# Performance work log

Hardware: AMD Instinct MI355X
Metric: run time of the kernel (lower is better)

## Reference

```python
import jax, jax.numpy as jnp
import numpy as np

B, L, D, K_LIN, T = 32, 512, 1024, 7, 8  # T = 1 identity ('root') + 7 linear experts


def setup_inputs() -> dict:
    key = jax.random.key(0)
    k0, k1, k2 = jax.random.split(key, 3)
    actions = jax.random.normal(k0, (B, L, D), dtype=jnp.float32)
    action_type = jax.random.randint(k1, (B, L), 0, T)
    W = jax.random.normal(k2, (K_LIN, D, D), dtype=jnp.float32) * 0.02  # (K, out, in)
    b = jnp.zeros((K_LIN, D), dtype=jnp.float32)
    return {"actions": actions, "action_type": action_type, "W": W, "b": b}


def reference(actions, action_type, W, b):
    # Project padded actions through ALL experts (matches original ModuleDict loop).
    # proj: (B, L, K_LIN, D) ; W is (K, out, in) so contract over input dim i.
    proj = jnp.einsum('bli,koi->blko', actions, W) + b[None, None, :, :]
    # 'root' expert is nn.Identity -> stacked first (dict insertion order).
    p = jnp.concatenate([actions[:, :, None, :], proj], axis=2)  # (B, L, T, D)
    # One-hot mask built via scatter in the original == one_hot here.
    mask = jax.nn.one_hot(action_type, T, dtype=p.dtype)[..., None]  # (B, L, T, 1)
    embedded = (mask * p).sum(axis=2)  # (B, L, D)
    return embedded
```

## Files before the change

kernel.cpp:

```cpp
#include <hip/hip_runtime.h>


#define NTOK 16384
#define DDIM 1024
#define NEXP 7
#define BM 256
#define BN 256
#define BK 64
#define NKT (DDIM / BK)

#define WI_OFFS   16
#define WI_NTILES 32
#define WI_TABLE  64
#define WI_CTOK   512
#define WS_ABF_B  1048576
#define WS_WBF_B  (WS_ABF_B + NTOK * DDIM * 2)

typedef __attribute__((ext_vector_type(8))) short short8;
typedef __attribute__((ext_vector_type(4))) float f32x4;

__device__ __forceinline__ unsigned short f2bf(float f) {
    unsigned u = __float_as_uint(f);
    u += 0x7fff + ((u >> 16) & 1);
    return (unsigned short)(u >> 16);
}

__device__ __forceinline__ void gload16(const void* g, void* l) {
    __builtin_amdgcn_global_load_lds(
        (const __attribute__((address_space(1))) void*)g,
        (__attribute__((address_space(3))) void*)l, 16, 0, 0);
}

__global__ __launch_bounds__(1024) void prep_k(
    const int* __restrict__ type, int* __restrict__ wsi,
    const float* __restrict__ W, unsigned short* __restrict__ Wbf,
    const float* __restrict__ A, unsigned short* __restrict__ Abf,
    float* __restrict__ out) {
    const int bid = blockIdx.x, tid = threadIdx.x;
    if (bid == 0) {
        __shared__ int h[16][8];
        __shared__ int base2[16][8];
        const int wave = tid >> 6, lane = tid & 63;
        const unsigned long long lt = (1ULL << lane) - 1;

        const int4* tsrc = (const int4*)(type + tid * 16);
        int4 v0 = tsrc[0], v1 = tsrc[1], v2 = tsrc[2], v3 = tsrc[3];
        int kv[16] = { v0.x, v0.y, v0.z, v0.w, v1.x, v1.y, v1.z, v1.w,
                       v2.x, v2.y, v2.z, v2.w, v3.x, v3.y, v3.z, v3.w };

        int cnt[8];
#pragma unroll
        for (int e = 0; e < 8; ++e) cnt[e] = 0;
#pragma unroll
        for (int i = 0; i < 16; ++i) {
#pragma unroll
            for (int e = 1; e < 8; ++e)
                cnt[e] += __popcll(__ballot(kv[i] == e));
        }
        if (lane == 0) {
#pragma unroll
            for (int e = 0; e < 8; ++e) h[wave][e] = cnt[e];
        }
        __syncthreads();

        if (tid == 0) {
            int acc = 0, t = 0;
            for (int e = 0; e < NEXP; ++e) {
                wsi[WI_OFFS + e] = acc;
                int run = acc;
                for (int w = 0; w < 16; ++w) { base2[w][e + 1] = run; run += h[w][e + 1]; }
                int nt = (run - acc + BM - 1) >> 8;
                for (int i = 0; i < nt; ++i) {
                    wsi[WI_TABLE + 2 * t] = e;
                    wsi[WI_TABLE + 2 * t + 1] = acc + i * BM;
                    ++t;
                }
                acc = run;
            }
            wsi[WI_OFFS + NEXP] = acc;
            wsi[WI_NTILES] = t;
        }
        __syncthreads();

        int rb[8];
#pragma unroll
        for (int e = 1; e < 8; ++e) rb[e] = base2[wave][e];
#pragma unroll
        for (int i = 0; i < 16; ++i) {
            int k = kv[i];
            int pos = -1;
#pragma unroll
            for (int e = 1; e < 8; ++e) {
                unsigned long long m = __ballot(k == e);
                int p = rb[e] + __popcll(m & lt);
                pos = (k == e) ? p : pos;
                rb[e] += __popcll(m);
            }
            if (k > 0) wsi[WI_CTOK + pos] = tid * 16 + i;
        }
    } else if (bid <= 448) {
        size_t i = ((size_t)(bid - 1) * 1024 + tid) * 16;
        const float4* src = (const float4*)(W + i);
        float4 v0 = src[0], v1 = src[1], v2 = src[2], v3 = src[3];
        short8 h0, h1;
        h0[0]=f2bf(v0.x); h0[1]=f2bf(v0.y); h0[2]=f2bf(v0.z); h0[3]=f2bf(v0.w);
        h0[4]=f2bf(v1.x); h0[5]=f2bf(v1.y); h0[6]=f2bf(v1.z); h0[7]=f2bf(v1.w);
        h1[0]=f2bf(v2.x); h1[1]=f2bf(v2.y); h1[2]=f2bf(v2.z); h1[3]=f2bf(v2.w);
        h1[4]=f2bf(v3.x); h1[5]=f2bf(v3.y); h1[6]=f2bf(v3.z); h1[7]=f2bf(v3.w);
        *(short8*)(Wbf + i) = h0;
        *(short8*)(Wbf + i + 8) = h1;
    } else {
        const int wave = tid >> 6, lane = tid & 63;
        const int t = (bid - 449) * 16 + wave;
        const float4* src = (const float4*)(A + (size_t)t * DDIM);
        if (type[t] == 0) {
            float4* d = (float4*)(out + (size_t)t * DDIM);
#pragma unroll
            for (int j = 0; j < 4; ++j) d[lane + j * 64] = src[lane + j * 64];
        } else {
            float4 v0 = src[lane * 4 + 0], v1 = src[lane * 4 + 1];
            float4 v2 = src[lane * 4 + 2], v3 = src[lane * 4 + 3];
            short8 h0, h1;
            h0[0]=f2bf(v0.x); h0[1]=f2bf(v0.y); h0[2]=f2bf(v0.z); h0[3]=f2bf(v0.w);
            h0[4]=f2bf(v1.x); h0[5]=f2bf(v1.y); h0[6]=f2bf(v1.z); h0[7]=f2bf(v1.w);
            h1[0]=f2bf(v2.x); h1[1]=f2bf(v2.y); h1[2]=f2bf(v2.z); h1[3]=f2bf(v2.w);
            h1[4]=f2bf(v3.x); h1[5]=f2bf(v3.y); h1[6]=f2bf(v3.z); h1[7]=f2bf(v3.w);
            unsigned short* d = Abf + (size_t)t * DDIM + lane * 16;
            *(short8*)d = h0;
            *(short8*)(d + 8) = h1;
        }
    }
}

#define TILE(Abase, Bbase, sNA, sNB, KT)                           \
    do {                                                           \
        short8 a1[8], b1[4];                                       \
        _Pragma("unroll")                                          \
        for (int m = 0; m < 8; ++m)                                \
            a1[m] = *(const short8*)(Abase + sl0 + m * 2048);      \
        _Pragma("unroll")                                          \
        for (int n = 0; n < 4; ++n)                                \
            b1[n] = *(const short8*)(Bbase + sl0 + n * 2048);      \
        if ((KT) + 1 < NKT) {                                      \
            const int ke_ = ((KT) + 1) * BK;                       \
            _Pragma("unroll")                                      \
            for (int q = 0; q < 4; ++q)                            \
                gload16(aSrc[q] + ke_, sNA + q * 8192);            \
            _Pragma("unroll")                                      \
            for (int q = 0; q < 4; ++q)                            \
                gload16(bSrc[q] + ke_, sNB + q * 8192);            \
        }                                                          \
        __builtin_amdgcn_s_setprio(1);                             \
        _Pragma("unroll")                                          \
        for (int m = 0; m < 8; ++m)                                \
            _Pragma("unroll")                                      \
            for (int n = 0; n < 4; ++n)                            \
                acc[m][n] = __builtin_amdgcn_mfma_f32_16x16x32_bf16(\
                    a1[m], b1[n], acc[m][n], 0, 0, 0);             \
        __builtin_amdgcn_s_setprio(0);                             \
        short8 a2[8], b2[4];                                       \
        _Pragma("unroll")                                          \
        for (int m = 0; m < 8; ++m)                                \
            a2[m] = *(const short8*)(Abase + sl1 + m * 2048);      \
        _Pragma("unroll")                                          \
        for (int n = 0; n < 4; ++n)                                \
            b2[n] = *(const short8*)(Bbase + sl1 + n * 2048);      \
        __builtin_amdgcn_s_setprio(1);                             \
        _Pragma("unroll")                                          \
        for (int m = 0; m < 8; ++m)                                \
            _Pragma("unroll")                                      \
            for (int n = 0; n < 4; ++n)                            \
                acc[m][n] = __builtin_amdgcn_mfma_f32_16x16x32_bf16(\
                    a2[m], b2[n], acc[m][n], 0, 0, 0);             \
        __builtin_amdgcn_s_setprio(0);                             \
        asm volatile("s_waitcnt vmcnt(0)" ::: "memory");           \
        __builtin_amdgcn_s_barrier();                              \
    } while (0)

__global__ __launch_bounds__(512, 2) void gemm_k(
    const unsigned short* __restrict__ Abf,
    const unsigned short* __restrict__ Wbf,
    const float* __restrict__ bias, float* __restrict__ out,
    const int* __restrict__ wsi) {
    const int bid = blockIdx.x;
    const int c = bid & 7;
    const int g = bid >> 3;
    const int ntiles = wsi[WI_NTILES];
    const int* offs = wsi + WI_OFFS;
    const int* tab  = wsi + WI_TABLE;
    const int* ctok = wsi + WI_CTOK;
    const int nlin  = offs[NEXP];

    __shared__ unsigned short As0[BM * BK];
    __shared__ unsigned short As1[BM * BK];
    __shared__ unsigned short Bs0[BM * BK];
    __shared__ unsigned short Bs1[BM * BK];

    const int tid = threadIdx.x, lane = tid & 63, wave = tid >> 6;
    const int wr = wave >> 2, wc = wave & 3;
    const int lane15 = lane & 15;
    const int srow = lane >> 3;
    const int schunk = ((lane & 7) ^ srow) * 8;

    const int sl0 = (((lane >> 4)) ^ (lane & 7)) * 16;
    const int sl1 = ((4 | (lane >> 4)) ^ (lane & 7)) * 16;
    const char* aR0 = (const char*)As0 + wr * 16384 + lane15 * 128;
    const char* aR1 = (const char*)As1 + wr * 16384 + lane15 * 128;
    const char* bR0 = (const char*)Bs0 + wc * 8192 + lane15 * 128;
    const char* bR1 = (const char*)Bs1 + wc * 8192 + lane15 * 128;
    char* sA0 = (char*)As0 + wave * 1024;
    char* sA1 = (char*)As1 + wave * 1024;
    char* sB0 = (char*)Bs0 + wave * 1024;
    char* sB1 = (char*)Bs1 + wave * 1024;

    for (int rep = 0; rep < 2; ++rep) {
        const int q4 = g + 32 * rep;
        const int ty = (q4 >> 2) * 8 + c;
        const int tx = q4 & 3;
        if (ty >= ntiles) break;

        const int e     = tab[2 * ty];
        const int crow0 = tab[2 * ty + 1];
        const int nend  = offs[e + 1];
        const int col0  = tx * BN;
        const unsigned short* Wb = Wbf + (size_t)e * DDIM * DDIM;

        const unsigned short* aSrc[4];
        const unsigned short* bSrc[4];
#pragma unroll
        for (int q = 0; q < 4; ++q) {
            int r = min(crow0 + q * 64 + wave * 8 + srow, nlin - 1);
            aSrc[q] = Abf + (size_t)ctok[r] * DDIM + schunk;
            bSrc[q] = Wb + (size_t)(col0 + q * 64 + wave * 8 + srow) * DDIM + schunk;
        }

        f32x4 acc[8][4];
#pragma unroll
        for (int m = 0; m < 8; ++m)
#pragma unroll
            for (int n = 0; n < 4; ++n) acc[m][n] = (f32x4){0.f, 0.f, 0.f, 0.f};

#pragma unroll
        for (int q = 0; q < 4; ++q) gload16(aSrc[q], sA0 + q * 8192);
#pragma unroll
        for (int q = 0; q < 4; ++q) gload16(bSrc[q], sB0 + q * 8192);
        asm volatile("s_waitcnt vmcnt(0)" ::: "memory");
        __builtin_amdgcn_s_barrier();

        for (int kt2 = 0; kt2 < NKT / 2; ++kt2) {
            TILE(aR0, bR0, sA1, sB1, 2 * kt2);
            TILE(aR1, bR1, sA0, sB0, 2 * kt2 + 1);
        }

        const int crow4 = (lane >> 4) * 4;
        float bv[4];
#pragma unroll
        for (int n = 0; n < 4; ++n)
            bv[n] = bias[e * DDIM + col0 + wc * 64 + n * 16 + lane15];

#pragma unroll
        for (int m = 0; m < 8; ++m) {
#pragma unroll
            for (int r = 0; r < 4; ++r) {
                int gr = crow0 + wr * 128 + m * 16 + crow4 + r;
                if (gr >= nend) continue;
                int tok = ctok[gr];
                float* orow = out + (size_t)tok * DDIM + col0 + wc * 64 + lane15;
#pragma unroll
                for (int n = 0; n < 4; ++n)
                    orow[n * 16] = acc[m][n][r] + bv[n];
            }
        }
        __builtin_amdgcn_s_barrier();
    }
}

extern "C" void kernel_launch(void* const* d_in, const int* in_sizes, int n_in,
                              void* d_out, int out_size, void* d_ws, size_t ws_size,
                              hipStream_t stream) {
    const float* actions = (const float*)d_in[0];
    const int*   atype   = (const int*)d_in[1];
    const float* W       = (const float*)d_in[2];
    const float* bias    = (const float*)d_in[3];
    float* out = (float*)d_out;

    int* wsi = (int*)d_ws;
    unsigned short* Abf = (unsigned short*)((char*)d_ws + WS_ABF_B);
    unsigned short* Wbf = (unsigned short*)((char*)d_ws + WS_WBF_B);

    prep_k<<<1473, 1024, 0, stream>>>(atype, wsi, W, Wbf, actions, Abf, out);
    gemm_k<<<256, 512, 0, stream>>>(Abf, Wbf, bias, out, wsi);
}
```

Measured before the change: 69.44 us.

## Restructure GEMM main loop into 4-phase pipeline with fine-grained staging

Replaces the two-half K-tile loop with four MFMA phases per tile, each covering a quadrant of the output (4 M-rows by 2 N-cols). Global-to-LDS loads are split into per-quadrant chunks that prefetch up to two tiles ahead, and partial vmcnt waits replace full drains. The aim is to overlap global loads, LDS reads and MFMA more finely and cut full-barrier stalls. It adds extra barriers per phase and relies on correct ordering of partial waits and buffer reuse across the two LDS buffers.

After: 73.10 us. 5.3% more time.

```diff
diff --git a/kernel.cpp b/kernel.cpp
--- a/kernel.cpp
+++ b/kernel.cpp
@@ -132,49 +132,65 @@
     }
 }
 
-#define TILE(Abase, Bbase, sNA, sNB, KT)                           \
-    do {                                                           \
-        short8 a1[8], b1[4];                                       \
-        _Pragma("unroll")                                          \
-        for (int m = 0; m < 8; ++m)                                \
-            a1[m] = *(const short8*)(Abase + sl0 + m * 2048);      \
-        _Pragma("unroll")                                          \
-        for (int n = 0; n < 4; ++n)                                \
-            b1[n] = *(const short8*)(Bbase + sl0 + n * 2048);      \
-        if ((KT) + 1 < NKT) {                                      \
-            const int ke_ = ((KT) + 1) * BK;                       \
-            _Pragma("unroll")                                      \
-            for (int q = 0; q < 4; ++q)                            \
-                gload16(aSrc[q] + ke_, sNA + q * 8192);            \
-            _Pragma("unroll")                                      \
-            for (int q = 0; q < 4; ++q)                            \
-                gload16(bSrc[q] + ke_, sNB + q * 8192);            \
-        }                                                          \
-        __builtin_amdgcn_s_setprio(1);                             \
-        _Pragma("unroll")                                          \
-        for (int m = 0; m < 8; ++m)                                \
-            _Pragma("unroll")                                      \
-            for (int n = 0; n < 4; ++n)                            \
-                acc[m][n] = __builtin_amdgcn_mfma_f32_16x16x32_bf16(\
-                    a1[m], b1[n], acc[m][n], 0, 0, 0);             \
-        __builtin_amdgcn_s_setprio(0);                             \
-        short8 a2[8], b2[4];                                       \
-        _Pragma("unroll")                                          \
-        for (int m = 0; m < 8; ++m)                                \
-            a2[m] = *(const short8*)(Abase + sl1 + m * 2048);      \
-        _Pragma("unroll")                                          \
-        for (int n = 0; n < 4; ++n)                                \
-            b2[n] = *(const short8*)(Bbase + sl1 + n * 2048);      \
-        __builtin_amdgcn_s_setprio(1);                             \
-        _Pragma("unroll")                                          \
-        for (int m = 0; m < 8; ++m)                                \
-            _Pragma("unroll")                                      \
-            for (int n = 0; n < 4; ++n)                            \
-                acc[m][n] = __builtin_amdgcn_mfma_f32_16x16x32_bf16(\
-                    a2[m], b2[n], acc[m][n], 0, 0, 0);             \
-        __builtin_amdgcn_s_setprio(0);                             \
-        asm volatile("s_waitcnt vmcnt(0)" ::: "memory");           \
-        __builtin_amdgcn_s_barrier();                              \
+#define RD_A(AR, MQ)                                                \
+    _Pragma("unroll")                                               \
+    for (int i = 0; i < 4; ++i) {                                   \
+        a[i][0] = *(const short8*)((AR) + ((MQ) * 4 + i) * 2048 + sl0); \
+        a[i][1] = *(const short8*)((AR) + ((MQ) * 4 + i) * 2048 + sl1); \
+    }
+
+#define RD_B(BR, NP)                                                \
+    _Pragma("unroll")                                               \
+    for (int n = 0; n < 2; ++n) {                                   \
+        b[n][0] = *(const short8*)((BR) + ((NP) * 2 + n) * 2048 + sl0); \
+        b[n][1] = *(const short8*)((BR) + ((NP) * 2 + n) * 2048 + sl1); \
+    }
+
+#define STG_A(DST, MQ, KTT)                                         \
+    gload16(aP[MQ][0] + (KTT) * BK, (char*)(DST) + dA[MQ][0]);      \
+    gload16(aP[MQ][1] + (KTT) * BK, (char*)(DST) + dA[MQ][1]);
+
+#define STG_B(DST, NP, KTT)                                         \
+    gload16(bP[NP][0] + (KTT) * BK, (char*)(DST) + dB[NP][0]);      \
+    gload16(bP[NP][1] + (KTT) * BK, (char*)(DST) + dB[NP][1]);
+
+#define MF_PH(MQ, NP)                                               \
+    __builtin_amdgcn_s_barrier();                                   \
+    asm volatile("s_waitcnt lgkmcnt(0)" ::: "memory");              \
+    __builtin_amdgcn_sched_barrier(0);                              \
+    __builtin_amdgcn_s_setprio(1);                                  \
+    _Pragma("unroll")                                               \
+    for (int i = 0; i < 4; ++i)                                     \
+        _Pragma("unroll")                                           \
+        for (int n = 0; n < 2; ++n) {                               \
+            acc[(MQ)*4+i][(NP)*2+n] = __builtin_amdgcn_mfma_f32_16x16x32_bf16( \
+                a[i][0], b[n][0], acc[(MQ)*4+i][(NP)*2+n], 0, 0, 0);\
+            acc[(MQ)*4+i][(NP)*2+n] = __builtin_amdgcn_mfma_f32_16x16x32_bf16( \
+                a[i][1], b[n][1], acc[(MQ)*4+i][(NP)*2+n], 0, 0, 0);\
+        }                                                           \
+    __builtin_amdgcn_s_setprio(0);                                  \
+    __builtin_amdgcn_s_barrier();
+
+#define TILE8(AR, BR, AD, BD, BDN, KT)                              \
+    do {                                                            \
+        short8 a[4][2], b[2][2];                                    \
+        RD_A(AR, 0); RD_B(BR, 0);                                   \
+        if ((KT) + 1 < NKT) { STG_B(BDN, 0, (KT) + 1); }            \
+        MF_PH(0, 0);                                                \
+        RD_B(BR, 1);                                                \
+        if ((KT) + 2 < NKT) { STG_A(AD, 0, (KT) + 2); }             \
+        MF_PH(0, 1);                                                \
+        RD_A(AR, 1);                                                \
+        if ((KT) + 2 < NKT) { STG_B(BD, 1, (KT) + 2); }             \
+        MF_PH(1, 1);                                                \
+        RD_B(BR, 0);                                                \
+        if ((KT) + 2 < NKT) {                                       \
+            STG_A(AD, 1, (KT) + 2);                                 \
+            asm volatile("s_waitcnt vmcnt(6)" ::: "memory");        \
+        } else {                                                    \
+            asm volatile("s_waitcnt vmcnt(0)" ::: "memory");        \
+        }                                                           \
+        MF_PH(1, 0);                                                \
     } while (0)
 
 __global__ __launch_bounds__(512, 2) void gemm_k(
@@ -199,8 +215,8 @@
     const int tid = threadIdx.x, lane = tid & 63, wave = tid >> 6;
     const int wr = wave >> 2, wc = wave & 3;
     const int lane15 = lane & 15;
-    const int srow = lane >> 3;
-    const int schunk = ((lane & 7) ^ srow) * 8;
+    const int l3 = lane >> 3;
+    const int schunk = ((lane & 7) ^ l3) * 8;
 
     const int sl0 = (((lane >> 4)) ^ (lane & 7)) * 16;
     const int sl1 = ((4 | (lane >> 4)) ^ (lane & 7)) * 16;
@@ -208,10 +224,18 @@
     const char* aR1 = (const char*)As1 + wr * 16384 + lane15 * 128;
     const char* bR0 = (const char*)Bs0 + wc * 8192 + lane15 * 128;
     const char* bR1 = (const char*)Bs1 + wc * 8192 + lane15 * 128;
-    char* sA0 = (char*)As0 + wave * 1024;
-    char* sA1 = (char*)As1 + wave * 1024;
-    char* sB0 = (char*)Bs0 + wave * 1024;
-    char* sB1 = (char*)Bs1 + wave * 1024;
+
+    int dA[2][2], dB[2][2];
+#pragma unroll
+    for (int mq = 0; mq < 2; ++mq)
+#pragma unroll
+        for (int j = 0; j < 2; ++j)
+            dA[mq][j] = (j * 128 + mq * 64 + wave * 8) * 128;
+#pragma unroll
+    for (int np = 0; np < 2; ++np)
+#pragma unroll
+        for (int j = 0; j < 2; ++j)
+            dB[np][j] = ((((wave >> 2) + 2 * j) * 64) + np * 32 + (wave & 3) * 8) * 128;
 
     for (int rep = 0; rep < 2; ++rep) {
         const int q4 = g + 32 * rep;
@@ -225,14 +249,17 @@
         const int col0  = tx * BN;
         const unsigned short* Wb = Wbf + (size_t)e * DDIM * DDIM;
 
-        const unsigned short* aSrc[4];
-        const unsigned short* bSrc[4];
-#pragma unroll
-        for (int q = 0; q < 4; ++q) {
-            int r = min(crow0 + q * 64 + wave * 8 + srow, nlin - 1);
-            aSrc[q] = Abf + (size_t)ctok[r] * DDIM + schunk;
-            bSrc[q] = Wb + (size_t)(col0 + q * 64 + wave * 8 + srow) * DDIM + schunk;
-        }
+        const unsigned short* aP[2][2];
+        const unsigned short* bP[2][2];
+#pragma unroll
+        for (int mq = 0; mq < 2; ++mq)
+#pragma unroll
+            for (int j = 0; j < 2; ++j) {
+                int r = j * 128 + mq * 64 + wave * 8 + l3;
+                aP[mq][j] = Abf + (size_t)ctok[min(crow0 + r, nlin - 1)] * DDIM + schunk;
+                int cc = ((wave >> 2) + 2 * j) * 64 + mq * 32 + (wave & 3) * 8 + l3;
+                bP[mq][j] = Wb + (size_t)(col0 + cc) * DDIM + schunk;
+            }
 
         f32x4 acc[8][4];
 #pragma unroll
@@ -240,16 +267,14 @@
 #pragma unroll
             for (int n = 0; n < 4; ++n) acc[m][n] = (f32x4){0.f, 0.f, 0.f, 0.f};
 
-#pragma unroll
-        for (int q = 0; q < 4; ++q) gload16(aSrc[q], sA0 + q * 8192);
-#pragma unroll
-        for (int q = 0; q < 4; ++q) gload16(bSrc[q], sB0 + q * 8192);
-        asm volatile("s_waitcnt vmcnt(0)" ::: "memory");
+        STG_A(As0, 0, 0); STG_B(Bs0, 0, 0); STG_B(Bs0, 1, 0); STG_A(As0, 1, 0);
+        STG_A(As1, 0, 1); STG_B(Bs1, 1, 1); STG_A(As1, 1, 1);
+        asm volatile("s_waitcnt vmcnt(6)" ::: "memory");
         __builtin_amdgcn_s_barrier();
 
         for (int kt2 = 0; kt2 < NKT / 2; ++kt2) {
-            TILE(aR0, bR0, sA1, sB1, 2 * kt2);
-            TILE(aR1, bR1, sA0, sB0, 2 * kt2 + 1);
+            TILE8(aR0, bR0, As0, Bs0, Bs1, 2 * kt2);
+            TILE8(aR1, bR1, As1, Bs1, Bs0, 2 * kt2 + 1);
         }
 
         const int crow4 = (lane >> 4) * 4;
```

## Fuse prep and grouped GEMM into one persistent kernel with grid barrier

Applied to the files above, without the earlier changes.

Merges the routing/conversion prep kernel and the grouped expert GEMM into a single 256-block kernel. Block 0 does the token bucketing, the other blocks grid-stride over the weight and activation bf16 conversion work, and then every block meets at an atomic grid-wide barrier before running the GEMM. This removes one kernel launch and the gap between the two kernels. In exchange it adds a memset for the barrier counter and relies on all 256 blocks being resident at once. The conversion phase now runs on far fewer threads (256x512 instead of 1473x1024), which may lower the memory bandwidth it reaches.

New measurement: 102.7 us. +47.9%, slower.

```diff
diff --git a/kernel.cpp b/kernel.cpp
--- a/kernel.cpp
+++ b/kernel.cpp
@@ -9,6 +9,7 @@
 #define BK 64
 #define NKT (DDIM / BK)
 
+#define WI_BAR    0
 #define WI_OFFS   16
 #define WI_NTILES 32
 #define WI_TABLE  64
@@ -29,107 +30,6 @@
     __builtin_amdgcn_global_load_lds(
         (const __attribute__((address_space(1))) void*)g,
         (__attribute__((address_space(3))) void*)l, 16, 0, 0);
-}
-
-__global__ __launch_bounds__(1024) void prep_k(
-    const int* __restrict__ type, int* __restrict__ wsi,
-    const float* __restrict__ W, unsigned short* __restrict__ Wbf,
-    const float* __restrict__ A, unsigned short* __restrict__ Abf,
-    float* __restrict__ out) {
-    const int bid = blockIdx.x, tid = threadIdx.x;
-    if (bid == 0) {
-        __shared__ int h[16][8];
-        __shared__ int base2[16][8];
-        const int wave = tid >> 6, lane = tid & 63;
-        const unsigned long long lt = (1ULL << lane) - 1;
-
-        const int4* tsrc = (const int4*)(type + tid * 16);
-        int4 v0 = tsrc[0], v1 = tsrc[1], v2 = tsrc[2], v3 = tsrc[3];
-        int kv[16] = { v0.x, v0.y, v0.z, v0.w, v1.x, v1.y, v1.z, v1.w,
-                       v2.x, v2.y, v2.z, v2.w, v3.x, v3.y, v3.z, v3.w };
-
-        int cnt[8];
-#pragma unroll
-        for (int e = 0; e < 8; ++e) cnt[e] = 0;
-#pragma unroll
-        for (int i = 0; i < 16; ++i) {
-#pragma unroll
-            for (int e = 1; e < 8; ++e)
-                cnt[e] += __popcll(__ballot(kv[i] == e));
-        }
-        if (lane == 0) {
-#pragma unroll
-            for (int e = 0; e < 8; ++e) h[wave][e] = cnt[e];
-        }
-        __syncthreads();
-
-        if (tid == 0) {
-            int acc = 0, t = 0;
-            for (int e = 0; e < NEXP; ++e) {
-                wsi[WI_OFFS + e] = acc;
-                int run = acc;
-                for (int w = 0; w < 16; ++w) { base2[w][e + 1] = run; run += h[w][e + 1]; }
-                int nt = (run - acc + BM - 1) >> 8;
-                for (int i = 0; i < nt; ++i) {
-                    wsi[WI_TABLE + 2 * t] = e;
-                    wsi[WI_TABLE + 2 * t + 1] = acc + i * BM;
-                    ++t;
-                }
-                acc = run;
-            }
-            wsi[WI_OFFS + NEXP] = acc;
-            wsi[WI_NTILES] = t;
-        }
-        __syncthreads();
-
-        int rb[8];
-#pragma unroll
-        for (int e = 1; e < 8; ++e) rb[e] = base2[wave][e];
-#pragma unroll
-        for (int i = 0; i < 16; ++i) {
-            int k = kv[i];
-            int pos = -1;
-#pragma unroll
-            for (int e = 1; e < 8; ++e) {
-                unsigned long long m = __ballot(k == e);
-                int p = rb[e] + __popcll(m & lt);
-                pos = (k == e) ? p : pos;
-                rb[e] += __popcll(m);
-            }
-            if (k > 0) wsi[WI_CTOK + pos] = tid * 16 + i;
-        }
-    } else if (bid <= 448) {
-        size_t i = ((size_t)(bid - 1) * 1024 + tid) * 16;
-        const float4* src = (const float4*)(W + i);
-        float4 v0 = src[0], v1 = src[1], v2 = src[2], v3 = src[3];
-        short8 h0, h1;
-        h0[0]=f2bf(v0.x); h0[1]=f2bf(v0.y); h0[2]=f2bf(v0.z); h0[3]=f2bf(v0.w);
-        h0[4]=f2bf(v1.x); h0[5]=f2bf(v1.y); h0[6]=f2bf(v1.z); h0[7]=f2bf(v1.w);
-        h1[0]=f2bf(v2.x); h1[1]=f2bf(v2.y); h1[2]=f2bf(v2.z); h1[3]=f2bf(v2.w);
-        h1[4]=f2bf(v3.x); h1[5]=f2bf(v3.y); h1[6]=f2bf(v3.z); h1[7]=f2bf(v3.w);
-        *(short8*)(Wbf + i) = h0;
-        *(short8*)(Wbf + i + 8) = h1;
-    } else {
-        const int wave = tid >> 6, lane = tid & 63;
-        const int t = (bid - 449) * 16 + wave;
-        const float4* src = (const float4*)(A + (size_t)t * DDIM);
-        if (type[t] == 0) {
-            float4* d = (float4*)(out + (size_t)t * DDIM);
-#pragma unroll
-            for (int j = 0; j < 4; ++j) d[lane + j * 64] = src[lane + j * 64];
-        } else {
-            float4 v0 = src[lane * 4 + 0], v1 = src[lane * 4 + 1];
-            float4 v2 = src[lane * 4 + 2], v3 = src[lane * 4 + 3];
-            short8 h0, h1;
-            h0[0]=f2bf(v0.x); h0[1]=f2bf(v0.y); h0[2]=f2bf(v0.z); h0[3]=f2bf(v0.w);
-            h0[4]=f2bf(v1.x); h0[5]=f2bf(v1.y); h0[6]=f2bf(v1.z); h0[7]=f2bf(v1.w);
-            h1[0]=f2bf(v2.x); h1[1]=f2bf(v2.y); h1[2]=f2bf(v2.z); h1[3]=f2bf(v2.w);
-            h1[4]=f2bf(v3.x); h1[5]=f2bf(v3.y); h1[6]=f2bf(v3.z); h1[7]=f2bf(v3.w);
-            unsigned short* d = Abf + (size_t)t * DDIM + lane * 16;
-            *(short8*)d = h0;
-            *(short8*)(d + 8) = h1;
-        }
-    }
 }
 
 #define TILE(Abase, Bbase, sNA, sNB, KT)                           \
@@ -177,12 +77,127 @@
         __builtin_amdgcn_s_barrier();                              \
     } while (0)
 
-__global__ __launch_bounds__(512, 2) void gemm_k(
-    const unsigned short* __restrict__ Abf,
-    const unsigned short* __restrict__ Wbf,
-    const float* __restrict__ bias, float* __restrict__ out,
-    const int* __restrict__ wsi) {
-    const int bid = blockIdx.x;
+__global__ __launch_bounds__(512, 2) void fused_k(
+    const int* __restrict__ type, int* __restrict__ wsi,
+    const float* __restrict__ W, unsigned short* __restrict__ Wbf,
+    const float* __restrict__ A, unsigned short* __restrict__ Abf,
+    const float* __restrict__ bias, float* __restrict__ out) {
+    const int bid = blockIdx.x, tid = threadIdx.x;
+    const int lane = tid & 63, wave = tid >> 6;
+
+    __shared__ unsigned short As0[BM * BK];
+    __shared__ unsigned short As1[BM * BK];
+    __shared__ unsigned short Bs0[BM * BK];
+    __shared__ unsigned short Bs1[BM * BK];
+    __shared__ int h[8][8];
+    __shared__ int base2[8][8];
+
+    if (bid == 0) {
+        const unsigned long long lt = (1ULL << lane) - 1;
+        const int4* tsrc = (const int4*)(type + tid * 32);
+        int4 v[8];
+#pragma unroll
+        for (int j = 0; j < 8; ++j) v[j] = tsrc[j];
+        int kv[32];
+#pragma unroll
+        for (int j = 0; j < 8; ++j) {
+            kv[4 * j + 0] = v[j].x; kv[4 * j + 1] = v[j].y;
+            kv[4 * j + 2] = v[j].z; kv[4 * j + 3] = v[j].w;
+        }
+        int cnt[8];
+#pragma unroll
+        for (int e = 0; e < 8; ++e) cnt[e] = 0;
+#pragma unroll
+        for (int i = 0; i < 32; ++i) {
+#pragma unroll
+            for (int e = 1; e < 8; ++e)
+                cnt[e] += __popcll(__ballot(kv[i] == e));
+        }
+        if (lane == 0) {
+#pragma unroll
+            for (int e = 0; e < 8; ++e) h[wave][e] = cnt[e];
+        }
+        __syncthreads();
+        if (tid == 0) {
+            int acc = 0, t = 0;
+            for (int e = 0; e < NEXP; ++e) {
+                wsi[WI_OFFS + e] = acc;
+                int run = acc;
+                for (int w = 0; w < 8; ++w) { base2[w][e + 1] = run; run += h[w][e + 1]; }
+                int nt = (run - acc + BM - 1) >> 8;
+                for (int i = 0; i < nt; ++i) {
+                    wsi[WI_TABLE + 2 * t] = e;
+                    wsi[WI_TABLE + 2 * t + 1] = acc + i * BM;
+                    ++t;
+                }
+                acc = run;
+            }
+            wsi[WI_OFFS + NEXP] = acc;
+            wsi[WI_NTILES] = t;
+        }
+        __syncthreads();
+        int rb[8];
+#pragma unroll
+        for (int e = 1; e < 8; ++e) rb[e] = base2[wave][e];
+#pragma unroll
+        for (int i = 0; i < 32; ++i) {
+            int k = kv[i];
+            int pos = -1;
+#pragma unroll
+            for (int e = 1; e < 8; ++e) {
+                unsigned long long m = __ballot(k == e);
+                int p = rb[e] + __popcll(m & lt);
+                pos = (k == e) ? p : pos;
+                rb[e] += __popcll(m);
+            }
+            if (k > 0) wsi[WI_CTOK + pos] = tid * 32 + i;
+        }
+    } else {
+        for (int u = bid - 1; u < 2944; u += 255) {
+            if (u < 896) {
+                size_t i = (size_t)u * 8192 + tid * 16;
+                const float4* src = (const float4*)(W + i);
+                float4 v0 = src[0], v1 = src[1], v2 = src[2], v3 = src[3];
+                short8 h0, h1;
+                h0[0]=f2bf(v0.x); h0[1]=f2bf(v0.y); h0[2]=f2bf(v0.z); h0[3]=f2bf(v0.w);
+                h0[4]=f2bf(v1.x); h0[5]=f2bf(v1.y); h0[6]=f2bf(v1.z); h0[7]=f2bf(v1.w);
+                h1[0]=f2bf(v2.x); h1[1]=f2bf(v2.y); h1[2]=f2bf(v2.z); h1[3]=f2bf(v2.w);
+                h1[4]=f2bf(v3.x); h1[5]=f2bf(v3.y); h1[6]=f2bf(v3.z); h1[7]=f2bf(v3.w);
+                *(short8*)(Wbf + i) = h0;
+                *(short8*)(Wbf + i + 8) = h1;
+            } else {
+                const int t = (u - 896) * 8 + wave;
+                const float4* src = (const float4*)(A + (size_t)t * DDIM);
+                if (type[t] == 0) {
+                    float4* d = (float4*)(out + (size_t)t * DDIM);
+#pragma unroll
+                    for (int j = 0; j < 4; ++j) d[lane + j * 64] = src[lane + j * 64];
+                } else {
+                    float4 v0 = src[lane * 4 + 0], v1 = src[lane * 4 + 1];
+                    float4 v2 = src[lane * 4 + 2], v3 = src[lane * 4 + 3];
+                    short8 h0, h1;
+                    h0[0]=f2bf(v0.x); h0[1]=f2bf(v0.y); h0[2]=f2bf(v0.z); h0[3]=f2bf(v0.w);
+                    h0[4]=f2bf(v1.x); h0[5]=f2bf(v1.y); h0[6]=f2bf(v1.z); h0[7]=f2bf(v1.w);
+                    h1[0]=f2bf(v2.x); h1[1]=f2bf(v2.y); h1[2]=f2bf(v2.z); h1[3]=f2bf(v2.w);
+                    h1[4]=f2bf(v3.x); h1[5]=f2bf(v3.y); h1[6]=f2bf(v3.z); h1[7]=f2bf(v3.w);
+                    unsigned short* d = Abf + (size_t)t * DDIM + lane * 16;
+                    *(short8*)d = h0;
+                    *(short8*)(d + 8) = h1;
+                }
+            }
+        }
+    }
+
+    __syncthreads();
+    if (tid == 0) {
+        __hip_atomic_fetch_add(&wsi[WI_BAR], 1, __ATOMIC_RELEASE,
+                               __HIP_MEMORY_SCOPE_AGENT);
+        while (__hip_atomic_load(&wsi[WI_BAR], __ATOMIC_ACQUIRE,
+                                 __HIP_MEMORY_SCOPE_AGENT) < 256)
+            __builtin_amdgcn_s_sleep(8);
+    }
+    __syncthreads();
+
     const int c = bid & 7;
     const int g = bid >> 3;
     const int ntiles = wsi[WI_NTILES];
@@ -191,12 +206,6 @@
     const int* ctok = wsi + WI_CTOK;
     const int nlin  = offs[NEXP];
 
-    __shared__ unsigned short As0[BM * BK];
-    __shared__ unsigned short As1[BM * BK];
-    __shared__ unsigned short Bs0[BM * BK];
-    __shared__ unsigned short Bs1[BM * BK];
-
-    const int tid = threadIdx.x, lane = tid & 63, wave = tid >> 6;
     const int wr = wave >> 2, wc = wave & 3;
     const int lane15 = lane & 15;
     const int srow = lane >> 3;
@@ -288,6 +297,7 @@
     unsigned short* Abf = (unsigned short*)((char*)d_ws + WS_ABF_B);
     unsigned short* Wbf = (unsigned short*)((char*)d_ws + WS_WBF_B);
 
-    prep_k<<<1473, 1024, 0, stream>>>(atype, wsi, W, Wbf, actions, Abf, out);
-    gemm_k<<<256, 512, 0, stream>>>(Abf, Wbf, bias, out, wsi);
+    hipMemsetAsync(d_ws, 0, 64, stream);
+    fused_k<<<256, 512, 0, stream>>>(atype, wsi, W, Wbf, actions, Abf,
+                                     bias, out);
 }
```

## Fuse activation bf16 conversion into GEMM A-tile loading

Applied to the files above, without the earlier changes.

Removes the separate pass in the prep kernel that converted gathered activations to a bf16 workspace buffer. The GEMM now reads fp32 activations directly into registers, converts them to bf16 and writes them into swizzled LDS, while B tiles still use direct global-to-LDS loads. This saves one fp32 read plus one bf16 write and read of the activation matrix. In exchange it adds register pressure (launch bounds drop to one block per CU), ALU conversion work and an extra LDS wait inside the main loop, and each A tile is re-read from global as fp32 by all four column-tile blocks.

Result: slower. 94.84 us (+36.6%).

```diff
diff --git a/kernel.cpp b/kernel.cpp
--- a/kernel.cpp
+++ b/kernel.cpp
@@ -13,8 +13,7 @@
 #define WI_NTILES 32
 #define WI_TABLE  64
 #define WI_CTOK   512
-#define WS_ABF_B  1048576
-#define WS_WBF_B  (WS_ABF_B + NTOK * DDIM * 2)
+#define WS_WBF_B  1048576
 
 typedef __attribute__((ext_vector_type(8))) short short8;
 typedef __attribute__((ext_vector_type(4))) float f32x4;
@@ -34,8 +33,7 @@
 __global__ __launch_bounds__(1024) void prep_k(
     const int* __restrict__ type, int* __restrict__ wsi,
     const float* __restrict__ W, unsigned short* __restrict__ Wbf,
-    const float* __restrict__ A, unsigned short* __restrict__ Abf,
-    float* __restrict__ out) {
+    const float* __restrict__ A, float* __restrict__ out) {
     const int bid = blockIdx.x, tid = threadIdx.x;
     if (bid == 0) {
         __shared__ int h[16][8];
@@ -112,29 +110,19 @@
     } else {
         const int wave = tid >> 6, lane = tid & 63;
         const int t = (bid - 449) * 16 + wave;
-        const float4* src = (const float4*)(A + (size_t)t * DDIM);
         if (type[t] == 0) {
+            const float4* src = (const float4*)(A + (size_t)t * DDIM);
             float4* d = (float4*)(out + (size_t)t * DDIM);
 #pragma unroll
             for (int j = 0; j < 4; ++j) d[lane + j * 64] = src[lane + j * 64];
-        } else {
-            float4 v0 = src[lane * 4 + 0], v1 = src[lane * 4 + 1];
-            float4 v2 = src[lane * 4 + 2], v3 = src[lane * 4 + 3];
-            short8 h0, h1;
-            h0[0]=f2bf(v0.x); h0[1]=f2bf(v0.y); h0[2]=f2bf(v0.z); h0[3]=f2bf(v0.w);
-            h0[4]=f2bf(v1.x); h0[5]=f2bf(v1.y); h0[6]=f2bf(v1.z); h0[7]=f2bf(v1.w);
-            h1[0]=f2bf(v2.x); h1[1]=f2bf(v2.y); h1[2]=f2bf(v2.z); h1[3]=f2bf(v2.w);
-            h1[4]=f2bf(v3.x); h1[5]=f2bf(v3.y); h1[6]=f2bf(v3.z); h1[7]=f2bf(v3.w);
-            unsigned short* d = Abf + (size_t)t * DDIM + lane * 16;
-            *(short8*)d = h0;
-            *(short8*)(d + 8) = h1;
         }
     }
 }
 
-#define TILE(Abase, Bbase, sNA, sNB, KT)                           \
+#define TILE(Abase, Bbase, dNA, sNB, KT)                           \
     do {                                                           \
         short8 a1[8], b1[4];                                       \
+        float4 fA[8];                                              \
         _Pragma("unroll")                                          \
         for (int m = 0; m < 8; ++m)                                \
             a1[m] = *(const short8*)(Abase + sl0 + m * 2048);      \
@@ -145,10 +133,13 @@
             const int ke_ = ((KT) + 1) * BK;                       \
             _Pragma("unroll")                                      \
             for (int q = 0; q < 4; ++q)                            \
-                gload16(aSrc[q] + ke_, sNA + q * 8192);            \
-            _Pragma("unroll")                                      \
-            for (int q = 0; q < 4; ++q)                            \
                 gload16(bSrc[q] + ke_, sNB + q * 8192);            \
+            _Pragma("unroll")                                      \
+            for (int q = 0; q < 4; ++q) {                          \
+                const float* p = aSrcF[q] + ke_;                   \
+                fA[2 * q]     = *(const float4*)p;                 \
+                fA[2 * q + 1] = *(const float4*)(p + 4);           \
+            }                                                      \
         }                                                          \
         __builtin_amdgcn_s_setprio(1);                             \
         _Pragma("unroll")                                          \
@@ -174,11 +165,23 @@
                     a2[m], b2[n], acc[m][n], 0, 0, 0);             \
         __builtin_amdgcn_s_setprio(0);                             \
         asm volatile("s_waitcnt vmcnt(0)" ::: "memory");           \
+        if ((KT) + 1 < NKT) {                                      \
+            _Pragma("unroll")                                      \
+            for (int q = 0; q < 4; ++q) {                          \
+                short8 w;                                          \
+                w[0]=f2bf(fA[2*q].x);   w[1]=f2bf(fA[2*q].y);      \
+                w[2]=f2bf(fA[2*q].z);   w[3]=f2bf(fA[2*q].w);      \
+                w[4]=f2bf(fA[2*q+1].x); w[5]=f2bf(fA[2*q+1].y);    \
+                w[6]=f2bf(fA[2*q+1].z); w[7]=f2bf(fA[2*q+1].w);    \
+                *(short8*)(dNA + awOff[q]) = w;                    \
+            }                                                      \
+            asm volatile("s_waitcnt lgkmcnt(0)" ::: "memory");     \
+        }                                                          \
         __builtin_amdgcn_s_barrier();                              \
     } while (0)
 
-__global__ __launch_bounds__(512, 2) void gemm_k(
-    const unsigned short* __restrict__ Abf,
+__global__ __launch_bounds__(512, 1) void gemm_k(
+    const float* __restrict__ Araw,
     const unsigned short* __restrict__ Wbf,
     const float* __restrict__ bias, float* __restrict__ out,
     const int* __restrict__ wsi) {
@@ -208,10 +211,14 @@
     const char* aR1 = (const char*)As1 + wr * 16384 + lane15 * 128;
     const char* bR0 = (const char*)Bs0 + wc * 8192 + lane15 * 128;
     const char* bR1 = (const char*)Bs1 + wc * 8192 + lane15 * 128;
-    char* sA0 = (char*)As0 + wave * 1024;
-    char* sA1 = (char*)As1 + wave * 1024;
     char* sB0 = (char*)Bs0 + wave * 1024;
     char* sB1 = (char*)Bs1 + wave * 1024;
+
+    int awOff[4];
+#pragma unroll
+    for (int q = 0; q < 4; ++q)
+        awOff[q] = (q * 64 + wave * 8 + srow) * 128 +
+                   (((lane & 7) ^ (srow & 7)) * 16);
 
     for (int rep = 0; rep < 2; ++rep) {
         const int q4 = g + 32 * rep;
@@ -225,12 +232,12 @@
         const int col0  = tx * BN;
         const unsigned short* Wb = Wbf + (size_t)e * DDIM * DDIM;
 
-        const unsigned short* aSrc[4];
+        const float* aSrcF[4];
         const unsigned short* bSrc[4];
 #pragma unroll
         for (int q = 0; q < 4; ++q) {
             int r = min(crow0 + q * 64 + wave * 8 + srow, nlin - 1);
-            aSrc[q] = Abf + (size_t)ctok[r] * DDIM + schunk;
+            aSrcF[q] = Araw + (size_t)ctok[r] * DDIM + (lane & 7) * 8;
             bSrc[q] = Wb + (size_t)(col0 + q * 64 + wave * 8 + srow) * DDIM + schunk;
         }
 
@@ -240,16 +247,32 @@
 #pragma unroll
             for (int n = 0; n < 4; ++n) acc[m][n] = (f32x4){0.f, 0.f, 0.f, 0.f};
 
-#pragma unroll
-        for (int q = 0; q < 4; ++q) gload16(aSrc[q], sA0 + q * 8192);
-#pragma unroll
-        for (int q = 0; q < 4; ++q) gload16(bSrc[q], sB0 + q * 8192);
-        asm volatile("s_waitcnt vmcnt(0)" ::: "memory");
-        __builtin_amdgcn_s_barrier();
+        {
+#pragma unroll
+            for (int q = 0; q < 4; ++q) gload16(bSrc[q], sB0 + q * 8192);
+            float4 fA[8];
+#pragma unroll
+            for (int q = 0; q < 4; ++q) {
+                fA[2 * q]     = *(const float4*)aSrcF[q];
+                fA[2 * q + 1] = *(const float4*)(aSrcF[q] + 4);
+            }
+            asm volatile("s_waitcnt vmcnt(0)" ::: "memory");
+#pragma unroll
+            for (int q = 0; q < 4; ++q) {
+                short8 w;
+                w[0]=f2bf(fA[2*q].x);   w[1]=f2bf(fA[2*q].y);
+                w[2]=f2bf(fA[2*q].z);   w[3]=f2bf(fA[2*q].w);
+                w[4]=f2bf(fA[2*q+1].x); w[5]=f2bf(fA[2*q+1].y);
+                w[6]=f2bf(fA[2*q+1].z); w[7]=f2bf(fA[2*q+1].w);
+                *(short8*)((char*)As0 + awOff[q]) = w;
+            }
+            asm volatile("s_waitcnt lgkmcnt(0)" ::: "memory");
+            __builtin_amdgcn_s_barrier();
+        }
 
         for (int kt2 = 0; kt2 < NKT / 2; ++kt2) {
-            TILE(aR0, bR0, sA1, sB1, 2 * kt2);
-            TILE(aR1, bR1, sA0, sB0, 2 * kt2 + 1);
+            TILE(aR0, bR0, (char*)As1, sB1, 2 * kt2);
+            TILE(aR1, bR1, (char*)As0, sB0, 2 * kt2 + 1);
         }
 
         const int crow4 = (lane >> 4) * 4;
@@ -285,9 +308,8 @@
     float* out = (float*)d_out;
 
     int* wsi = (int*)d_ws;
-    unsigned short* Abf = (unsigned short*)((char*)d_ws + WS_ABF_B);
     unsigned short* Wbf = (unsigned short*)((char*)d_ws + WS_WBF_B);
 
-    prep_k<<<1473, 1024, 0, stream>>>(atype, wsi, W, Wbf, actions, Abf, out);
-    gemm_k<<<256, 512, 0, stream>>>(Abf, Wbf, bias, out, wsi);
-}
+    prep_k<<<1473, 1024, 0, stream>>>(atype, wsi, W, Wbf, actions, out);
+    gemm_k<<<256, 512, 0, stream>>>(actions, Wbf, bias, out, wsi);
+}
```
